# Performance work log

Measured on AMD Instinct MI355X. Metric: run time of the kernel, lower is better.

## Reference

```python
import jax, jax.numpy as jnp
import numpy as np

B, T, D = 4, 4096, 1024
H = 16
DK = D // H
EPS = 1e-6


def _phi(x):
    return jax.nn.elu(x) + 1.0


def setup_inputs() -> dict:
    key = jax.random.key(0)
    ks = jax.random.split(key, 9)
    s = 1.0 / np.sqrt(D)
    return {
        "x": jax.random.normal(ks[0], (B, T, D), dtype=jnp.float32),
        "Wq": jax.random.uniform(ks[1], (D, D), jnp.float32, -s, s),
        "bq": jax.random.uniform(ks[2], (D,), jnp.float32, -s, s),
        "Wk": jax.random.uniform(ks[3], (D, D), jnp.float32, -s, s),
        "bk": jax.random.uniform(ks[4], (D,), jnp.float32, -s, s),
        "Wv": jax.random.uniform(ks[5], (D, D), jnp.float32, -s, s),
        "bv": jax.random.uniform(ks[6], (D,), jnp.float32, -s, s),
        "Wo": jax.random.uniform(ks[7], (D, D), jnp.float32, -s, s),
        "bo": jax.random.uniform(ks[8], (D,), jnp.float32, -s, s),
    }


def reference(x, Wq, bq, Wk, bk, Wv, bv, Wo, bo):
    Bq, Tq, _ = x.shape

    def heads(y):  # [B,T,D] -> [B,H,T,DK]
        return y.reshape(Bq, Tq, H, DK).transpose(0, 2, 1, 3)

    q = _phi(heads(x @ Wq.T + bq))
    k = _phi(heads(x @ Wk.T + bk))
    v = heads(x @ Wv.T + bv)

    # associative KV summary: [B,H,DK,DK]
    kv = jnp.einsum("bhtd,bhtm->bhdm", k, v)
    # normalizer: q . (sum_t k + eps), then +eps, reciprocal
    z = 1.0 / (jnp.einsum("bhtd,bhd->bht", q, k.sum(axis=2) + EPS) + EPS)
    out = jnp.einsum("bhtd,bhdm,bht->bhtm", q, kv, z)

    out = out.transpose(0, 2, 1, 3).reshape(Bq, Tq, -1)  # [B,T,D]
    return out @ Wo.T + bo
```

## Files before the change

kernel.cpp:

```cpp
#include <hip/hip_runtime.h>
#include <cstdint>
#include <cstddef>

typedef unsigned short u16;
typedef __bf16 bf16x8 __attribute__((ext_vector_type(8)));
typedef float  f32x4  __attribute__((ext_vector_type(4)));
typedef u16    u16x8v __attribute__((ext_vector_type(8)));
typedef u16    u16x4  __attribute__((ext_vector_type(4)));

#define EPS 1e-6f

__device__ __forceinline__ u16 f2bf(float f) {
  union { float f; unsigned int u; } v; v.f = f;
  unsigned int u = v.u + 0x7FFFu + ((v.u >> 16) & 1u);
  return (u16)(u >> 16);
}
__device__ __forceinline__ float bf2f(u16 h) {
  union { unsigned int u; float f; } v; v.u = ((unsigned int)h) << 16;
  return v.f;
}
__device__ __forceinline__ void async16(const void* g, void* l) {
  __builtin_amdgcn_global_load_lds(
      (const __attribute__((address_space(1))) void*)g,
      (__attribute__((address_space(3))) void*)l, 16, 0, 0);
}

__global__ __launch_bounds__(256) void cvt_bf16_kernel(
    const float* __restrict__ in, u16* __restrict__ out, int n8) {
  int i = blockIdx.x * 256 + threadIdx.x;
  if (i >= n8) return;
  const float4* p = (const float4*)in;
  float4 a = p[2 * (size_t)i], b = p[2 * (size_t)i + 1];
  u16x8v o;
  o[0] = f2bf(a.x); o[1] = f2bf(a.y); o[2] = f2bf(a.z); o[3] = f2bf(a.w);
  o[4] = f2bf(b.x); o[5] = f2bf(b.y); o[6] = f2bf(b.z); o[7] = f2bf(b.w);
  *(u16x8v*)(out + 8 * (size_t)i) = o;
}

__global__ __launch_bounds__(256) void cvt_w_kernel(
    const float* __restrict__ w0, const float* __restrict__ w1,
    const float* __restrict__ w2, const float* __restrict__ w3,
    u16* __restrict__ o0, u16* __restrict__ o1,
    u16* __restrict__ o2, u16* __restrict__ o3) {
  const int gb = blockIdx.x;
  const float* in = (gb < 512) ? w0 : (gb < 1024) ? w1 : (gb < 1536) ? w2 : w3;
  u16* out = (gb < 512) ? o0 : (gb < 1024) ? o1 : (gb < 1536) ? o2 : o3;
  const int i = (gb & 511) * 256 + threadIdx.x;
  const float4* p = (const float4*)in;
  float4 a = p[2 * (size_t)i], b = p[2 * (size_t)i + 1];
  u16x8v o;
  o[0] = f2bf(a.x); o[1] = f2bf(a.y); o[2] = f2bf(a.z); o[3] = f2bf(a.w);
  o[4] = f2bf(b.x); o[5] = f2bf(b.y); o[6] = f2bf(b.z); o[7] = f2bf(b.w);
  *(u16x8v*)(out + 8 * (size_t)i) = o;
}

template <int MODE>
__global__ __launch_bounds__(512) void gemm8g(
    const u16* __restrict__ A, const u16* __restrict__ Bw,
    const float* __restrict__ bias0, const float* __restrict__ bias1,
    const float* __restrict__ bias2,
    u16* __restrict__ O0, u16* __restrict__ O1, u16* __restrict__ O2,
    float* __restrict__ Of, int K) {
  __shared__ u16 sA[2][256 * 64];
  __shared__ u16 sB[2][256 * 64];

  const int tid = threadIdx.x, wave = tid >> 6, lane = tid & 63;
  const int bm = blockIdx.x * 256, bn = blockIdx.y * 256;
  const int wmh = (wave >> 2) * 64;
  const int wq  = (wave & 3) * 32;
  const int l15 = lane & 15, l4 = lane >> 4, l7 = lane & 7;

  f32x4 acc[8][4] = {};

  const int trow = tid >> 3;
  const int sch8 = ((tid & 7) ^ (trow & 7)) * 8;

#define STG_A(buf, qm, s, kt)                                                 \
  async16(A + (size_t)(bm + (s)*128 + (qm)*64 + trow) * K + (kt) + sch8,      \
          &sA[buf][(((qm)*128 + (s)*64) + wave * 8) * 64])
#define STG_B(buf, qn, s, kt)                                                 \
  async16(Bw + (size_t)(bn + ((s)*2 + (trow >> 5)) * 64 + (qn)*32 +           \
                        (trow & 31)) * K + (kt) + sch8,                       \
          &sB[buf][(((qn)*128 + (s)*64) + wave * 8) * 64])

  bf16x8 af[4][2], bq[2][2];

#define RD_A(buf, qm)                                                         \
  _Pragma("unroll") for (int m = 0; m < 4; m++)                               \
    _Pragma("unroll") for (int kk = 0; kk < 2; kk++)                          \
      af[m][kk] = *(const bf16x8*)&sA[buf][((qm)*128 + wmh + m * 16 + l15) * 64 \
                                           + ((kk * 4 + l4) ^ l7) * 8];
#define RD_B(buf, qn)                                                         \
  _Pragma("unroll") for (int f = 0; f < 2; f++)                               \
    _Pragma("unroll") for (int kk = 0; kk < 2; kk++)                          \
      bq[f][kk] = *(const bf16x8*)&sB[buf][((qn)*128 + wq + f * 16 + l15) * 64 \
                                           + ((kk * 4 + l4) ^ l7) * 8];

#define WAITV_(n) asm volatile("s_waitcnt vmcnt(" #n ")" ::: "memory")
#define WAITV(n) WAITV_(n)

#define PH(qm, qn, W)                                                         \
  __builtin_amdgcn_s_barrier();                                               \
  asm volatile("s_waitcnt lgkmcnt(0)" ::: "memory");                          \
  __builtin_amdgcn_sched_barrier(0);                                          \
  __builtin_amdgcn_s_setprio(1);                                              \
  _Pragma("unroll") for (int kk = 0; kk < 2; kk++)                            \
    _Pragma("unroll") for (int m = 0; m < 4; m++)                             \
      _Pragma("unroll") for (int n = 0; n < 2; n++)                           \
        acc[(qm)*4 + m][(qn)*2 + n] = __builtin_amdgcn_mfma_f32_16x16x32_bf16(\
            af[m][kk], bq[n][kk], acc[(qm)*4 + m][(qn)*2 + n], 0, 0, 0);      \
  __builtin_amdgcn_s_setprio(0);                                              \
  WAITV(W);                                                                   \
  __builtin_amdgcn_s_barrier();                                               \
  asm volatile("" ::: "memory");

#define ITER8(kO, kE2, kO2, FULL, W0, W1, W2, W3, W4, W5, W6, W7)             \
                                                   \
  RD_A(0, 0); RD_B(0, 0);                                                     \
  STG_B(1, 0, 0, kO); STG_B(1, 0, 1, kO);                \
  PH(0, 0, W0);                                                               \
                                                          \
  RD_B(0, 1);                                                                 \
  if (FULL) { STG_A(0, 0, 0, kE2); STG_A(0, 0, 1, kE2); }          \
  PH(0, 1, W1);                                                               \
                                                          \
  RD_A(0, 1);                                                                 \
  if (FULL) { STG_B(0, 1, 0, kE2); STG_B(0, 1, 1, kE2); }          \
  PH(1, 1, W2);                                                               \
                                                          \
  RD_B(0, 0);                                                                 \
  if (FULL) { STG_A(0, 1, 0, kE2); STG_A(0, 1, 1, kE2); }          \
  PH(1, 0, W3);                                                               \
                                                   \
  RD_A(1, 0); RD_B(1, 0);                                                     \
  if (FULL) { STG_B(0, 0, 0, kE2); STG_B(0, 0, 1, kE2); }          \
  PH(0, 0, W4);                                                               \
                                                          \
  RD_B(1, 1);                                                                 \
  if (FULL) { STG_A(1, 0, 0, kO2); STG_A(1, 0, 1, kO2); }          \
  PH(0, 1, W5);                                                               \
                                                          \
  RD_A(1, 1);                                                                 \
  if (FULL) { STG_B(1, 1, 0, kO2); STG_B(1, 1, 1, kO2); }          \
  PH(1, 1, W6);                                                               \
                                                          \
  RD_B(1, 0);                                                                 \
  if (FULL) { STG_A(1, 1, 0, kO2); STG_A(1, 1, 1, kO2); }          \
  PH(1, 0, W7);

  STG_A(0, 0, 0, 0);  STG_A(0, 0, 1, 0);
  STG_B(0, 0, 0, 0);  STG_B(0, 0, 1, 0);
  STG_B(0, 1, 0, 0);  STG_B(0, 1, 1, 0);
  STG_A(0, 1, 0, 0);  STG_A(0, 1, 1, 0);
  STG_A(1, 0, 0, 64); STG_A(1, 0, 1, 64);
  STG_B(1, 1, 0, 64); STG_B(1, 1, 1, 64);
  STG_A(1, 1, 0, 64); STG_A(1, 1, 1, 64);
  WAITV(10);
  __builtin_amdgcn_s_barrier();
  asm volatile("" ::: "memory");

  const int NT = K >> 6;
  const int NI = NT >> 1;
  ITER8(64, 128, 192, true, 10, 10, 12, 12, 12, 12, 12, 12);
  for (int i = 1; i < NI - 1; ++i) {
    const int kO  = (2 * i + 1) * 64;
    const int kE2 = (2 * i + 2) * 64;
    const int kO2 = (2 * i + 3) * 64;
    ITER8(kO, kE2, kO2, true, 12, 12, 12, 12, 12, 12, 12, 12);
  }
  ITER8((NT - 1) * 64, 0, 0, false, 12, 10, 8, 6, 4, 2, 0, 0);
#undef STG_A
#undef STG_B
#undef RD_A
#undef RD_B
#undef WAITV
#undef WAITV_
#undef PH
#undef ITER8

  const int wm = wmh * 2;
  const int wn = (wave & 3) * 64;
  const int r0 = l4 * 4, cc = l15;
  if constexpr (MODE == 1) {
    const int mat = blockIdx.y >> 2;
    u16* outp = (mat == 0) ? O0 : (mat == 1) ? O1 : O2;
    const float* bias = (mat == 0) ? bias0 : (mat == 1) ? bias1 : bias2;
    const int act = (mat < 2);
    const int colb = (blockIdx.y & 3) * 256;
    float bvv[4];
#pragma unroll
    for (int ni = 0; ni < 4; ni++) bvv[ni] = bias[colb + wn + ni * 16 + cc];
#pragma unroll
    for (int mi = 0; mi < 8; mi++) {
#pragma unroll
      for (int j = 0; j < 4; j++) {
        const int row = bm + wm + mi * 16 + r0 + j;
#pragma unroll
        for (int ni = 0; ni < 4; ni++) {
          const int col = colb + wn + ni * 16 + cc;
          float val = acc[mi][ni][j] + bvv[ni];
          if (act) val = (val > 0.f) ? (val + 1.f) : __expf(val);
          outp[(size_t)row * 1024 + col] = f2bf(val);
        }
      }
    }
  } else {
    float bvv[4];
#pragma unroll
    for (int ni = 0; ni < 4; ni++) bvv[ni] = bias0[bn + wn + ni * 16 + cc];
#pragma unroll
    for (int mi = 0; mi < 8; mi++) {
#pragma unroll
      for (int j = 0; j < 4; j++) {
        const int row = bm + wm + mi * 16 + r0 + j;
#pragma unroll
        for (int ni = 0; ni < 4; ni++) {
          const int col = bn + wn + ni * 16 + cc;
          Of[(size_t)row * 1024 + col] = acc[mi][ni][j] + bvv[ni];
        }
      }
    }
  }
}

__global__ __launch_bounds__(256) void kv_mfma_kernel(
    const u16* __restrict__ Kb, const u16* __restrict__ Vb,
    float* __restrict__ kv, float* __restrict__ ksum) {
  const int bh = blockIdx.y;
  const int chunk = blockIdx.x;
  const int b = bh >> 4, h = bh & 15;
  const int tid = threadIdx.x, wave = tid >> 6, lane = tid & 63;

  __shared__ u16 sKT[64 * 64];
  __shared__ u16 sVT[64 * 64];

  f32x4 acc[4] = {};
  f32x4 accs[4] = {};

  union { u16x8v u; bf16x8 b; } uo;
#pragma unroll
  for (int e = 0; e < 8; e++) uo.u[e] = 0x3F80;
  const bf16x8 ones = uo.b;

  const int half = tid >> 7;
  const int j    = tid & 127;
  const int tg   = j >> 3;
  const int dg   = j & 7;
  const u16* src = half ? Vb : Kb;
  u16* dst = half ? sVT : sKT;
  const int colb = (4 * tg + 8 * dg) & 63;

  const size_t rowBase = (size_t)b * 4096 + (size_t)chunk * 512;
  const size_t gbase = (rowBase + 4 * tg) * 1024 + (size_t)h * 64 + dg * 8;

  u16x8v pre[2][4];
#pragma unroll
  for (int s = 0; s < 4; s++)
    pre[0][s] = *(const u16x8v*)(src + gbase + (size_t)s * 1024);

#pragma unroll
  for (int st = 0; st < 8; st++) {
    const int cb = st & 1;
    __syncthreads();
#pragma unroll
    for (int e = 0; e < 8; e++) {
      u16x4 w;
      w[0] = pre[cb][0][e]; w[1] = pre[cb][1][e];
      w[2] = pre[cb][2][e]; w[3] = pre[cb][3][e];
      *(u16x4*)&dst[(dg * 8 + e) * 64 + colb] = w;
    }
    if (st + 1 < 8) {
      const size_t nb = gbase + (size_t)(st + 1) * 64 * 1024;
#pragma unroll
      for (int s = 0; s < 4; s++)
        pre[cb ^ 1][s] = *(const u16x8v*)(src + nb + (size_t)s * 1024);
    }
    __syncthreads();

#pragma unroll
    for (int kst = 0; kst < 2; kst++) {
      const int q8 = kst * 32 + (lane >> 4) * 8;
      bf16x8 bfrag;
      {
        const int rr = wave * 16 + (lane & 15);
        const int c = (q8 + 8 * (rr >> 3)) & 63;
        bfrag = *(const bf16x8*)&sVT[rr * 64 + c];
      }
#pragma unroll
      for (int i = 0; i < 4; i++) {
        const int rr = i * 16 + (lane & 15);
        const int c = (q8 + 8 * (rr >> 3)) & 63;
        const bf16x8 afrag = *(const bf16x8*)&sKT[rr * 64 + c];
        acc[i] = __builtin_amdgcn_mfma_f32_16x16x32_bf16(afrag, bfrag, acc[i], 0, 0, 0);
        if (wave == 0)
          accs[i] = __builtin_amdgcn_mfma_f32_16x16x32_bf16(afrag, ones, accs[i], 0, 0, 0);
      }
    }
  }

  const int r0 = (lane >> 4) * 4, cc = lane & 15;
  float* kvp = kv + (size_t)bh * 4096;
#pragma unroll
  for (int i = 0; i < 4; i++)
#pragma unroll
    for (int jj = 0; jj < 4; jj++)
      atomicAdd(&kvp[(size_t)(i * 16 + r0 + jj) * 64 + wave * 16 + cc], acc[i][jj]);
  if (wave == 0 && cc == 0) {
#pragma unroll
    for (int i = 0; i < 4; i++)
#pragma unroll
      for (int jj = 0; jj < 4; jj++)
        atomicAdd(&ksum[(size_t)bh * 64 + i * 16 + r0 + jj], accs[i][jj]);
  }
}

#define QST 80
__global__ __launch_bounds__(256) void attn_apply_kernel(
    const u16* __restrict__ Qb, const float* __restrict__ kv,
    const float* __restrict__ ksum, u16* __restrict__ attn) {
  const int bh = blockIdx.y;
  const int tt = blockIdx.x;
  const int b = bh >> 4, h = bh & 15;
  const int tid = threadIdx.x, wave = tid >> 6, lane = tid & 63;

  __shared__ u16 skvT[64 * QST];
  __shared__ u16 sq[64 * QST];
  __shared__ float sz[64];
  __shared__ float sks[64];

  if (tid < 64) sks[tid] = ksum[(size_t)bh * 64 + tid] + EPS;

  const float* kvp = kv + (size_t)bh * 4096;
  for (int i = tid; i < 4096; i += 256) {
    const int dd = i >> 6, mm = i & 63;
    skvT[mm * QST + dd] = f2bf(kvp[i]);
  }
  const size_t qbase = ((size_t)b * 4096 + (size_t)tt * 64) * 1024 + h * 64;
  for (int i = tid; i < 4096; i += 256) {
    const int r = i >> 6, dd = i & 63;
    sq[r * QST + dd] = Qb[qbase + (size_t)r * 1024 + dd];
  }
  __syncthreads();

  if (tid < 64) {
    float za = 0.f;
#pragma unroll
    for (int j = 0; j < 64; j++) {
      const int dd = (j + tid) & 63;
      za += bf2f(sq[tid * QST + dd]) * sks[dd];
    }
    sz[tid] = 1.f / (za + EPS);
  }
  __syncthreads();

  f32x4 acc[4] = {};
#pragma unroll
  for (int ks2 = 0; ks2 < 2; ks2++) {
    const bf16x8 a = *(const bf16x8*)&sq[(wave * 16 + (lane & 15)) * QST + ks2 * 32 + (lane >> 4) * 8];
#pragma unroll
    for (int ni = 0; ni < 4; ni++) {
      const bf16x8 bv = *(const bf16x8*)&skvT[(ni * 16 + (lane & 15)) * QST + ks2 * 32 + (lane >> 4) * 8];
      acc[ni] = __builtin_amdgcn_mfma_f32_16x16x32_bf16(a, bv, acc[ni], 0, 0, 0);
    }
  }

  const int r0 = (lane >> 4) * 4, cc = lane & 15;
#pragma unroll
  for (int ni = 0; ni < 4; ni++) {
#pragma unroll
    for (int j = 0; j < 4; j++) {
      const int r = wave * 16 + r0 + j;
      const int c = ni * 16 + cc;
      const float val = acc[ni][j] * sz[r];
      attn[qbase + (size_t)r * 1024 + c] = f2bf(val);
    }
  }
}

extern "C" void kernel_launch(void* const* d_in, const int* in_sizes, int n_in,
                              void* d_out, int out_size, void* d_ws, size_t ws_size,
                              hipStream_t stream) {
  (void)in_sizes; (void)n_in; (void)out_size; (void)ws_size;
  const float* x  = (const float*)d_in[0];
  const float* Wq = (const float*)d_in[1];
  const float* bq = (const float*)d_in[2];
  const float* Wk = (const float*)d_in[3];
  const float* bk = (const float*)d_in[4];
  const float* Wv = (const float*)d_in[5];
  const float* bv = (const float*)d_in[6];
  const float* Wo = (const float*)d_in[7];
  const float* bo = (const float*)d_in[8];

  char* ws = (char*)d_ws;
  u16* xb    = (u16*)ws;  ws += 33554432;
  u16* wqkvb = (u16*)ws;  ws += 6291456;
  u16* wob   = (u16*)ws;  ws += 2097152;
  u16* Vb    = (u16*)ws;  ws += 33554432;
  u16* attn  = (u16*)ws;  ws += 33554432;
  float* kvb  = (float*)ws; ws += 1048576;
  float* ksum = (float*)ws; ws += 16384;

  u16* Qb = (u16*)d_out;
  u16* Kb = Qb + 16777216;

  hipMemsetAsync(kvb, 0, 1048576 + 16384, stream);

  cvt_bf16_kernel<<<8192, 256, 0, stream>>>(x, xb, 2097152);
  cvt_w_kernel<<<2048, 256, 0, stream>>>(Wq, Wk, Wv, Wo,
                                         wqkvb, wqkvb + 1048576, wqkvb + 2097152, wob);

  gemm8g<1><<<dim3(64, 12), 512, 0, stream>>>(
      xb, wqkvb, bq, bk, bv, Qb, Kb, Vb, nullptr, 1024);

  kv_mfma_kernel<<<dim3(8, 64), dim3(256), 0, stream>>>(Kb, Vb, kvb, ksum);
  attn_apply_kernel<<<dim3(64, 64), dim3(256), 0, stream>>>(Qb, kvb, ksum, attn);

  gemm8g<0><<<dim3(64, 4), 512, 0, stream>>>(
      attn, wob, bo, nullptr, nullptr, nullptr, nullptr, nullptr,
      (float*)d_out, 1024);
}
```

Measured before the change: 327.2 us.

## Replace KV atomics with partial sums plus reduce kernel, retune GEMM waits

The KV summary kernel now writes per-chunk partial results instead of using atomicAdd, and a new reduce kernel sums the 8 chunks and converts KV to bf16 once. This removes the memset and the atomic contention, and it stops each of the 64 attention blocks per head from converting the fp32 KV itself. The attention kernel also spreads the normalizer dot product across all 256 threads instead of 64. Separately, the GEMM pipeline's vmcnt wait thresholds are changed at two phases per iteration, which could also alter correctness margins of the async load pipeline. Costs are one extra kernel launch and the extra partial-buffer traffic.

```diff
diff --git a/kernel.cpp b/kernel.cpp
--- a/kernel.cpp
+++ b/kernel.cpp
@@ -115,35 +115,27 @@
   asm volatile("" ::: "memory");
 
 #define ITER8(kO, kE2, kO2, FULL, W0, W1, W2, W3, W4, W5, W6, W7)             \
-                                                   \
   RD_A(0, 0); RD_B(0, 0);                                                     \
   STG_B(1, 0, 0, kO); STG_B(1, 0, 1, kO);                \
   PH(0, 0, W0);                                                               \
-                                                          \
   RD_B(0, 1);                                                                 \
   if (FULL) { STG_A(0, 0, 0, kE2); STG_A(0, 0, 1, kE2); }          \
   PH(0, 1, W1);                                                               \
-                                                          \
   RD_A(0, 1);                                                                 \
   if (FULL) { STG_B(0, 1, 0, kE2); STG_B(0, 1, 1, kE2); }          \
   PH(1, 1, W2);                                                               \
-                                                          \
   RD_B(0, 0);                                                                 \
   if (FULL) { STG_A(0, 1, 0, kE2); STG_A(0, 1, 1, kE2); }          \
   PH(1, 0, W3);                                                               \
-                                                   \
   RD_A(1, 0); RD_B(1, 0);                                                     \
   if (FULL) { STG_B(0, 0, 0, kE2); STG_B(0, 0, 1, kE2); }          \
   PH(0, 0, W4);                                                               \
-                                                          \
   RD_B(1, 1);                                                                 \
   if (FULL) { STG_A(1, 0, 0, kO2); STG_A(1, 0, 1, kO2); }          \
   PH(0, 1, W5);                                                               \
-                                                          \
   RD_A(1, 1);                                                                 \
   if (FULL) { STG_B(1, 1, 0, kO2); STG_B(1, 1, 1, kO2); }          \
   PH(1, 1, W6);                                                               \
-                                                          \
   RD_B(1, 0);                                                                 \
   if (FULL) { STG_A(1, 1, 0, kO2); STG_A(1, 1, 1, kO2); }          \
   PH(1, 0, W7);
@@ -161,14 +153,14 @@
 
   const int NT = K >> 6;
   const int NI = NT >> 1;
-  ITER8(64, 128, 192, true, 10, 10, 12, 12, 12, 12, 12, 12);
+  ITER8(64, 128, 192, true, 10, 10, 12, 6, 12, 12, 12, 6);
   for (int i = 1; i < NI - 1; ++i) {
     const int kO  = (2 * i + 1) * 64;
     const int kE2 = (2 * i + 2) * 64;
     const int kO2 = (2 * i + 3) * 64;
-    ITER8(kO, kE2, kO2, true, 12, 12, 12, 12, 12, 12, 12, 12);
-  }
-  ITER8((NT - 1) * 64, 0, 0, false, 12, 10, 8, 6, 4, 2, 0, 0);
+    ITER8(kO, kE2, kO2, true, 12, 12, 12, 6, 12, 12, 12, 6);
+  }
+  ITER8((NT - 1) * 64, 0, 0, false, 12, 12, 12, 0, 0, 0, 0, 0);
 #undef STG_A
 #undef STG_B
 #undef RD_A
@@ -225,7 +217,7 @@
 
 __global__ __launch_bounds__(256) void kv_mfma_kernel(
     const u16* __restrict__ Kb, const u16* __restrict__ Vb,
-    float* __restrict__ kv, float* __restrict__ ksum) {
+    float* __restrict__ kv_part, float* __restrict__ ksum_part) {
   const int bh = blockIdx.y;
   const int chunk = blockIdx.x;
   const int b = bh >> 4, h = bh & 15;
@@ -299,24 +291,51 @@
   }
 
   const int r0 = (lane >> 4) * 4, cc = lane & 15;
-  float* kvp = kv + (size_t)bh * 4096;
+  float* kvp = kv_part + ((size_t)chunk * 64 + bh) * 4096;
 #pragma unroll
   for (int i = 0; i < 4; i++)
 #pragma unroll
     for (int jj = 0; jj < 4; jj++)
-      atomicAdd(&kvp[(size_t)(i * 16 + r0 + jj) * 64 + wave * 16 + cc], acc[i][jj]);
+      kvp[(size_t)(i * 16 + r0 + jj) * 64 + wave * 16 + cc] = acc[i][jj];
   if (wave == 0 && cc == 0) {
 #pragma unroll
     for (int i = 0; i < 4; i++)
 #pragma unroll
       for (int jj = 0; jj < 4; jj++)
-        atomicAdd(&ksum[(size_t)bh * 64 + i * 16 + r0 + jj], accs[i][jj]);
+        ksum_part[((size_t)chunk * 64 + bh) * 64 + i * 16 + r0 + jj] = accs[i][jj];
+  }
+}
+
+__global__ __launch_bounds__(256) void kv_reduce_kernel(
+    const float* __restrict__ kv_part, const float* __restrict__ ksum_part,
+    u16* __restrict__ kvbf, float* __restrict__ ksum) {
+  const int bh = blockIdx.x;
+  const int tid = threadIdx.x;
+#pragma unroll
+  for (int it = 0; it < 4; it++) {
+    const int idx = it * 1024 + tid * 4;
+    float4 s = {0.f, 0.f, 0.f, 0.f};
+#pragma unroll
+    for (int c = 0; c < 8; c++) {
+      const float4 p = *(const float4*)&kv_part[((size_t)c * 64 + bh) * 4096 + idx];
+      s.x += p.x; s.y += p.y; s.z += p.z; s.w += p.w;
+    }
+    u16x4 o;
+    o[0] = f2bf(s.x); o[1] = f2bf(s.y); o[2] = f2bf(s.z); o[3] = f2bf(s.w);
+    *(u16x4*)&kvbf[(size_t)bh * 4096 + idx] = o;
+  }
+  if (tid < 64) {
+    float s = 0.f;
+#pragma unroll
+    for (int c = 0; c < 8; c++)
+      s += ksum_part[((size_t)c * 64 + bh) * 64 + tid];
+    ksum[(size_t)bh * 64 + tid] = s;
   }
 }
 
 #define QST 80
 __global__ __launch_bounds__(256) void attn_apply_kernel(
-    const u16* __restrict__ Qb, const float* __restrict__ kv,
+    const u16* __restrict__ Qb, const u16* __restrict__ kvbf,
     const float* __restrict__ ksum, u16* __restrict__ attn) {
   const int bh = blockIdx.y;
   const int tt = blockIdx.x;
@@ -327,13 +346,14 @@
   __shared__ u16 sq[64 * QST];
   __shared__ float sz[64];
   __shared__ float sks[64];
+  __shared__ float szp[256];
 
   if (tid < 64) sks[tid] = ksum[(size_t)bh * 64 + tid] + EPS;
 
-  const float* kvp = kv + (size_t)bh * 4096;
+  const u16* kvp = kvbf + (size_t)bh * 4096;
   for (int i = tid; i < 4096; i += 256) {
     const int dd = i >> 6, mm = i & 63;
-    skvT[mm * QST + dd] = f2bf(kvp[i]);
+    skvT[mm * QST + dd] = kvp[i];
   }
   const size_t qbase = ((size_t)b * 4096 + (size_t)tt * 64) * 1024 + h * 64;
   for (int i = tid; i < 4096; i += 256) {
@@ -342,15 +362,19 @@
   }
   __syncthreads();
 
-  if (tid < 64) {
-    float za = 0.f;
-#pragma unroll
-    for (int j = 0; j < 64; j++) {
-      const int dd = (j + tid) & 63;
-      za += bf2f(sq[tid * QST + dd]) * sks[dd];
-    }
-    sz[tid] = 1.f / (za + EPS);
-  }
+  {
+    const int zr = tid & 63, zg = tid >> 6;
+    float pz = 0.f;
+#pragma unroll
+    for (int jj = 0; jj < 16; jj++) {
+      const int dd = zg * 16 + jj;
+      pz += bf2f(sq[zr * QST + dd]) * sks[dd];
+    }
+    szp[zg * 64 + zr] = pz;
+  }
+  __syncthreads();
+  if (tid < 64)
+    sz[tid] = 1.f / (szp[tid] + szp[64 + tid] + szp[128 + tid] + szp[192 + tid] + EPS);
   __syncthreads();
 
   f32x4 acc[4] = {};
@@ -397,13 +421,13 @@
   u16* wob   = (u16*)ws;  ws += 2097152;
   u16* Vb    = (u16*)ws;  ws += 33554432;
   u16* attn  = (u16*)ws;  ws += 33554432;
-  float* kvb  = (float*)ws; ws += 1048576;
-  float* ksum = (float*)ws; ws += 16384;
+  float* kv_part   = (float*)ws; ws += 8388608;
+  float* ksum_part = (float*)ws; ws += 131072;
+  u16*   kvbf      = (u16*)ws;   ws += 524288;
+  float* ksum      = (float*)ws; ws += 16384;
 
   u16* Qb = (u16*)d_out;
   u16* Kb = Qb + 16777216;
-
-  hipMemsetAsync(kvb, 0, 1048576 + 16384, stream);
 
   cvt_bf16_kernel<<<8192, 256, 0, stream>>>(x, xb, 2097152);
   cvt_w_kernel<<<2048, 256, 0, stream>>>(Wq, Wk, Wv, Wo,
@@ -412,8 +436,9 @@
   gemm8g<1><<<dim3(64, 12), 512, 0, stream>>>(
       xb, wqkvb, bq, bk, bv, Qb, Kb, Vb, nullptr, 1024);
 
-  kv_mfma_kernel<<<dim3(8, 64), dim3(256), 0, stream>>>(Kb, Vb, kvb, ksum);
-  attn_apply_kernel<<<dim3(64, 64), dim3(256), 0, stream>>>(Qb, kvb, ksum, attn);
+  kv_mfma_kernel<<<dim3(8, 64), dim3(256), 0, stream>>>(Kb, Vb, kv_part, ksum_part);
+  kv_reduce_kernel<<<64, 256, 0, stream>>>(kv_part, ksum_part, kvbf, ksum);
+  attn_apply_kernel<<<dim3(64, 64), dim3(256), 0, stream>>>(Qb, kvbf, ksum, attn);
 
   gemm8g<0><<<dim3(64, 4), 512, 0, stream>>>(
       attn, wob, bo, nullptr, nullptr, nullptr, nullptr, nullptr,
```

New measurement: 318.7 us. 2.6% less time.
